# Performance work log

Measured on AMD Instinct MI355X. Metric: run time of the kernel, lower is better.

Reference implementation:

```python
import jax, jax.numpy as jnp
import numpy as np

D_MODEL = 2048
N_HEADS = 16
HEAD_DIM = D_MODEL // N_HEADS
ROPE_BASE = 10000.0


def rope_cos_sin(seq_len, head_dim, dtype=jnp.float32):
    inv_freq = 1.0 / (ROPE_BASE ** (jnp.arange(0, head_dim, 2, dtype=jnp.float32) / head_dim))
    pos = jnp.arange(seq_len, dtype=jnp.float32)
    freqs = pos[:, None] * inv_freq[None, :]          # [S, head_dim/2]
    emb = jnp.concatenate([freqs, freqs], axis=-1)    # [S, head_dim]
    return jnp.cos(emb).astype(dtype), jnp.sin(emb).astype(dtype)


def rotate_half(x):
    x1, x2 = jnp.split(x, 2, axis=-1)
    return jnp.concatenate([-x2, x1], axis=-1)


def apply_rope(x, cos, sin):
    # x: [B, S, H, hd]; cos/sin: [S, hd] broadcast over batch and heads
    c = cos[None, :, None, :]
    s = sin[None, :, None, :]
    return x * c + rotate_half(x) * s


def setup_inputs() -> dict:
    key = jax.random.key(0)
    kx, kq, kk, kv, ko = jax.random.split(key, 5)
    B, S = 4, 2048
    scale = 1.0 / np.sqrt(D_MODEL)
    x = jax.random.normal(kx, (B, S, D_MODEL), dtype=jnp.float32)
    Wq = jax.random.normal(kq, (D_MODEL, D_MODEL), dtype=jnp.float32) * scale
    Wk = jax.random.normal(kk, (D_MODEL, D_MODEL), dtype=jnp.float32) * scale
    Wv = jax.random.normal(kv, (D_MODEL, D_MODEL), dtype=jnp.float32) * scale
    Wo = jax.random.normal(ko, (D_MODEL, D_MODEL), dtype=jnp.float32) * scale
    return {"x": x, "Wq": Wq, "Wk": Wk, "Wv": Wv, "Wo": Wo}


def reference(x, Wq, Wk, Wv, Wo):
    B, S, D = x.shape
    H, hd = N_HEADS, HEAD_DIM
    # QKV projections (torch Linear: y = x @ W.T)
    q = jnp.einsum('bsd,ed->bse', x, Wq).reshape(B, S, H, hd)
    k = jnp.einsum('bsd,ed->bse', x, Wk).reshape(B, S, H, hd)
    v = jnp.einsum('bsd,ed->bse', x, Wv).reshape(B, S, H, hd)
    # RoPE (no past cache -> positions 0..S-1 for both Q and K)
    cos, sin = rope_cos_sin(S, hd, x.dtype)
    q = apply_rope(q, cos, sin)
    k = apply_rope(k, cos, sin)
    # Scaled dot-product attention, causal (training path with mask=None)
    scores = jnp.einsum('bqhd,bkhd->bhqk', q, k) / jnp.sqrt(jnp.asarray(hd, x.dtype))
    causal = jnp.tril(jnp.ones((S, S), dtype=bool))
    scores = jnp.where(causal[None, None], scores, jnp.asarray(-jnp.inf, scores.dtype))
    attn = jax.nn.softmax(scores, axis=-1)
    out = jnp.einsum('bhqk,bkhd->bqhd', attn, v).reshape(B, S, D)
    return jnp.einsum('bsd,ed->bse', out, Wo)
```

## Files before the change

kernel.cpp:

```cpp
#include <hip/hip_runtime.h>
#include <stdint.h>

#define DMODEL 2048
#define NHEADS 16
#define HD     128
#define BATCH  4
#define SEQ    2048
#define MROWS  (BATCH*SEQ)

typedef __attribute__((ext_vector_type(8))) short short8;
typedef __attribute__((ext_vector_type(4))) float f32x4;

__device__ __forceinline__ unsigned short f2bf(float f) {
  uint32_t u = __float_as_uint(f);
  u += 0x7FFFu + ((u >> 16) & 1u);
  return (unsigned short)(u >> 16);
}
__device__ __forceinline__ float bf2f(unsigned short s) {
  return __uint_as_float(((uint32_t)s) << 16);
}

__global__ __launch_bounds__(256) void cvt_f32_bf16(
    const float* __restrict__ src, unsigned short* __restrict__ dst, int n4) {
  int i = blockIdx.x * 256 + threadIdx.x;
  if (i >= n4) return;
  float4 f = ((const float4*)src)[i];
  ushort4 o;
  o.x = f2bf(f.x); o.y = f2bf(f.y); o.z = f2bf(f.z); o.w = f2bf(f.w);
  ((ushort4*)dst)[i] = o;
}

__global__ __launch_bounds__(256) void rope_table(
    float* __restrict__ ct, float* __restrict__ st) {
  int idx = blockIdx.x * 256 + threadIdx.x;
  int s = idx >> 6, i = idx & 63;
  float invf = exp2f(-(float)i * (13.287712379549449f / 64.0f));
  float a = (float)s * invf;
  ct[idx] = cosf(a);
  st[idx] = sinf(a);
}

__global__ __launch_bounds__(256) void rope_apply(
    unsigned short* __restrict__ X, const float* __restrict__ ct,
    const float* __restrict__ st) {
  int idx = blockIdx.x * 256 + threadIdx.x;
  int i0  = (idx & 15) * 4;
  int h   = (idx >> 4) & 15;
  int row = idx >> 8;
  int s   = row & (SEQ - 1);
  size_t base = (size_t)row * DMODEL + h * HD + i0;
  ushort4 lo = *(const ushort4*)&X[base];
  ushort4 hi = *(const ushort4*)&X[base + 64];
  float4 c  = *(const float4*)&ct[s * 64 + i0];
  float4 sn = *(const float4*)&st[s * 64 + i0];
  ushort4 olo, ohi;
  olo.x = f2bf(bf2f(lo.x) * c.x - bf2f(hi.x) * sn.x);
  olo.y = f2bf(bf2f(lo.y) * c.y - bf2f(hi.y) * sn.y);
  olo.z = f2bf(bf2f(lo.z) * c.z - bf2f(hi.z) * sn.z);
  olo.w = f2bf(bf2f(lo.w) * c.w - bf2f(hi.w) * sn.w);
  ohi.x = f2bf(bf2f(hi.x) * c.x + bf2f(lo.x) * sn.x);
  ohi.y = f2bf(bf2f(hi.y) * c.y + bf2f(lo.y) * sn.y);
  ohi.z = f2bf(bf2f(hi.z) * c.z + bf2f(lo.z) * sn.z);
  ohi.w = f2bf(bf2f(hi.w) * c.w + bf2f(lo.w) * sn.w);
  *(ushort4*)&X[base]      = olo;
  *(ushort4*)&X[base + 64] = ohi;
}

template<bool OUT_BF16>
__global__ __launch_bounds__(256) void gemm_nt(
    const unsigned short* __restrict__ A,
    const unsigned short* __restrict__ B0, const unsigned short* __restrict__ B1,
    const unsigned short* __restrict__ B2,
    void* __restrict__ C0, void* __restrict__ C1, void* __restrict__ C2,
    int K, int N) {
  const unsigned short* Bm = (blockIdx.z == 0) ? B0 : (blockIdx.z == 1) ? B1 : B2;
  void* Cm = (blockIdx.z == 0) ? C0 : (blockIdx.z == 1) ? C1 : C2;
  const int m0 = blockIdx.x * 128, n0 = blockIdx.y * 128;
  __shared__ unsigned short As[128 * 64];
  __shared__ unsigned short Bs[128 * 64];
  const int t = threadIdx.x, w = t >> 6, lane = t & 63;
  const int wr = w >> 1, wc = w & 1, g = lane >> 4, cl = lane & 15;

  f32x4 acc[4][4];
  const f32x4 zero = {0.f, 0.f, 0.f, 0.f};
#pragma unroll
  for (int mi = 0; mi < 4; ++mi)
#pragma unroll
    for (int ni = 0; ni < 4; ++ni) acc[mi][ni] = zero;

  for (int k0 = 0; k0 < K; k0 += 64) {
    __syncthreads();
#pragma unroll
    for (int i = 0; i < 4; ++i) {
      int f16 = (w * 4 + i) * 64 + lane;
      int row = f16 >> 3, col = (f16 & 7) * 8;
      __builtin_amdgcn_global_load_lds(
          (const __attribute__((address_space(1))) void*)(A + (size_t)(m0 + row) * K + k0 + col),
          (__attribute__((address_space(3))) void*)(&As[(size_t)f16 * 8]), 16, 0, 0);
      __builtin_amdgcn_global_load_lds(
          (const __attribute__((address_space(1))) void*)(Bm + (size_t)(n0 + row) * K + k0 + col),
          (__attribute__((address_space(3))) void*)(&Bs[(size_t)f16 * 8]), 16, 0, 0);
    }
    __syncthreads();
#pragma unroll
    for (int kk = 0; kk < 2; ++kk) {
      short8 a[4], b[4];
#pragma unroll
      for (int mi = 0; mi < 4; ++mi)
        a[mi] = *(const short8*)&As[(wr * 64 + mi * 16 + cl) * 64 + kk * 32 + g * 8];
#pragma unroll
      for (int ni = 0; ni < 4; ++ni)
        b[ni] = *(const short8*)&Bs[(wc * 64 + ni * 16 + cl) * 64 + kk * 32 + g * 8];
#pragma unroll
      for (int mi = 0; mi < 4; ++mi)
#pragma unroll
        for (int ni = 0; ni < 4; ++ni)
          acc[mi][ni] = __builtin_amdgcn_mfma_f32_16x16x32_bf16(a[mi], b[ni], acc[mi][ni], 0, 0, 0);
    }
  }
#pragma unroll
  for (int mi = 0; mi < 4; ++mi)
#pragma unroll
    for (int ni = 0; ni < 4; ++ni) {
      int row = m0 + wr * 64 + mi * 16 + g * 4;
      int col = n0 + wc * 64 + ni * 16 + cl;
#pragma unroll
      for (int r = 0; r < 4; ++r) {
        float v = acc[mi][ni][r];
        if (OUT_BF16)
          ((unsigned short*)Cm)[(size_t)(row + r) * N + col] = f2bf(v);
        else
          ((float*)Cm)[(size_t)(row + r) * N + col] = v;
      }
    }
}

__global__ __launch_bounds__(256) void attn_kernel(
    const unsigned short* __restrict__ Q, const unsigned short* __restrict__ Kk,
    const unsigned short* __restrict__ V, unsigned short* __restrict__ O) {
  const int qt = (int)gridDim.x - 1 - (int)blockIdx.x;
  const int q0 = qt * 64;
  const int bh = blockIdx.y, b = bh >> 4, h = bh & 15;
  const size_t base = (size_t)b * SEQ * DMODEL + (size_t)h * HD;

  __shared__ unsigned short Ks[64 * 136];
  __shared__ unsigned short Vt[128 * 72];
  __shared__ unsigned short Pl[4][16 * 72];

  const int t = threadIdx.x, w = t >> 6, lane = t & 63;
  const int g = lane >> 4, cl = lane & 15;

  short8 qf[4];
  {
    const unsigned short* qrow = Q + base + (size_t)(q0 + w * 16 + cl) * DMODEL;
#pragma unroll
    for (int kk = 0; kk < 4; ++kk) qf[kk] = *(const short8*)(qrow + kk * 32 + g * 8);
  }

  f32x4 o_acc[8];
  const f32x4 zero = {0.f, 0.f, 0.f, 0.f};
#pragma unroll
  for (int n = 0; n < 8; ++n) o_acc[n] = zero;
  float m_run[4], l_run[4];
#pragma unroll
  for (int r = 0; r < 4; ++r) { m_run[r] = -INFINITY; l_run[r] = 0.f; }

  const int my_qmax = q0 + w * 16 + 15;
  const int ntiles = qt + 1;
  constexpr float SC = 0.08838834764831845f * 1.4426950408889634f;

  for (int tkv = 0; tkv < ntiles; ++tkv) {
    const int kv0 = tkv * 64;
    __syncthreads();
#pragma unroll
    for (int p = 0; p < 4; ++p) {
      int row = p * 16 + (t >> 4), c8 = t & 15;
      const unsigned short* src = Kk + base + (size_t)(kv0 + row) * DMODEL + c8 * 8;
      *(short8*)&Ks[row * 136 + c8 * 8] = *(const short8*)src;
    }
#pragma unroll
    for (int p = 0; p < 4; ++p) {
      int kv = t & 63, h0 = ((t >> 6) + p * 4) * 8;
      const unsigned short* src = V + base + (size_t)(kv0 + kv) * DMODEL + h0;
      short8 vv = *(const short8*)src;
#pragma unroll
      for (int e = 0; e < 8; ++e) Vt[(h0 + e) * 72 + kv] = (unsigned short)vv[e];
    }
    __syncthreads();

    if (kv0 <= my_qmax) {
      float sm[4][4];
#pragma unroll
      for (int c = 0; c < 4; ++c) {
        f32x4 sa = zero;
#pragma unroll
        for (int kk = 0; kk < 4; ++kk) {
          short8 kf = *(const short8*)&Ks[(c * 16 + cl) * 136 + kk * 32 + g * 8];
          sa = __builtin_amdgcn_mfma_f32_16x16x32_bf16(qf[kk], kf, sa, 0, 0, 0);
        }
#pragma unroll
        for (int r = 0; r < 4; ++r) {
          float sv = sa[r] * SC;
          int kvg = kv0 + c * 16 + cl;
          int qg  = q0 + w * 16 + g * 4 + r;
          sm[c][r] = (kvg > qg) ? -INFINITY : sv;
        }
      }
      float alpha[4];
#pragma unroll
      for (int r = 0; r < 4; ++r) {
        float mx = fmaxf(fmaxf(sm[0][r], sm[1][r]), fmaxf(sm[2][r], sm[3][r]));
#pragma unroll
        for (int msk = 8; msk >= 1; msk >>= 1) mx = fmaxf(mx, __shfl_xor(mx, msk, 16));
        float mnew = fmaxf(m_run[r], mx);
        alpha[r] = exp2f(m_run[r] - mnew);
        m_run[r] = mnew;
        float s0 = 0.f;
#pragma unroll
        for (int c = 0; c < 4; ++c) {
          float p = exp2f(sm[c][r] - mnew);
          sm[c][r] = p;
          s0 += p;
        }
#pragma unroll
        for (int msk = 8; msk >= 1; msk >>= 1) s0 += __shfl_xor(s0, msk, 16);
        l_run[r] = l_run[r] * alpha[r] + s0;
      }
#pragma unroll
      for (int n = 0; n < 8; ++n)
#pragma unroll
        for (int r = 0; r < 4; ++r) o_acc[n][r] *= alpha[r];
#pragma unroll
      for (int c = 0; c < 4; ++c)
#pragma unroll
        for (int r = 0; r < 4; ++r)
          Pl[w][(g * 4 + r) * 72 + c * 16 + cl] = f2bf(sm[c][r]);
#pragma unroll
      for (int kk = 0; kk < 2; ++kk) {
        short8 pa = *(const short8*)&Pl[w][cl * 72 + kk * 32 + g * 8];
#pragma unroll
        for (int n = 0; n < 8; ++n) {
          short8 vf = *(const short8*)&Vt[(n * 16 + cl) * 72 + kk * 32 + g * 8];
          o_acc[n] = __builtin_amdgcn_mfma_f32_16x16x32_bf16(pa, vf, o_acc[n], 0, 0, 0);
        }
      }
    }
  }
  {
    const size_t obase = base + (size_t)(q0 + w * 16) * DMODEL;
#pragma unroll
    for (int r = 0; r < 4; ++r) {
      float inv = 1.0f / l_run[r];
      int qrow = g * 4 + r;
#pragma unroll
      for (int n = 0; n < 8; ++n)
        O[obase + (size_t)qrow * DMODEL + n * 16 + cl] = f2bf(o_acc[n][r] * inv);
    }
  }
}

extern "C" void kernel_launch(void* const* d_in, const int* in_sizes, int n_in,
                              void* d_out, int out_size, void* d_ws, size_t ws_size,
                              hipStream_t stream) {
  const float* x  = (const float*)d_in[0];
  const float* Wq = (const float*)d_in[1];
  const float* Wk = (const float*)d_in[2];
  const float* Wv = (const float*)d_in[3];
  const float* Wo = (const float*)d_in[4];
  float* out = (float*)d_out;

  unsigned short* wsb = (unsigned short*)d_ws;
  const size_t XN = (size_t)MROWS * DMODEL;
  const size_t WN = (size_t)DMODEL * DMODEL;
  unsigned short* xb  = wsb;
  unsigned short* wqb = xb  + XN;
  unsigned short* wkb = wqb + WN;
  unsigned short* wvb = wkb + WN;
  unsigned short* wob = wvb + WN;
  unsigned short* qb  = wob + WN;
  unsigned short* kb  = qb  + XN;
  unsigned short* vb  = kb  + XN;
  unsigned short* aob = vb  + XN;
  float* cost = (float*)(aob + XN);
  float* sint = cost + (size_t)SEQ * 64;

  cvt_f32_bf16<<<(int)(XN / 4 / 256), 256, 0, stream>>>(x,  xb,  (int)(XN / 4));
  cvt_f32_bf16<<<(int)(WN / 4 / 256), 256, 0, stream>>>(Wq, wqb, (int)(WN / 4));
  cvt_f32_bf16<<<(int)(WN / 4 / 256), 256, 0, stream>>>(Wk, wkb, (int)(WN / 4));
  cvt_f32_bf16<<<(int)(WN / 4 / 256), 256, 0, stream>>>(Wv, wvb, (int)(WN / 4));
  cvt_f32_bf16<<<(int)(WN / 4 / 256), 256, 0, stream>>>(Wo, wob, (int)(WN / 4));

  rope_table<<<(SEQ * 64) / 256, 256, 0, stream>>>(cost, sint);

  gemm_nt<true><<<dim3(MROWS / 128, DMODEL / 128, 3), 256, 0, stream>>>(
      xb, wqb, wkb, wvb, (void*)qb, (void*)kb, (void*)vb, DMODEL, DMODEL);

  rope_apply<<<(MROWS * NHEADS * 16) / 256, 256, 0, stream>>>(qb, cost, sint);
  rope_apply<<<(MROWS * NHEADS * 16) / 256, 256, 0, stream>>>(kb, cost, sint);

  attn_kernel<<<dim3(SEQ / 64, BATCH * NHEADS), 256, 0, stream>>>(qb, kb, vb, aob);

  gemm_nt<false><<<dim3(MROWS / 128, DMODEL / 128, 1), 256, 0, stream>>>(
      aob, wob, wob, wob, (void*)out, (void*)out, (void*)out, DMODEL, DMODEL);
}
```

Measured before the change: 996.8 us.

## Pre-transpose V, use direct global-to-LDS loads with swizzle, double Q tile

Adds a separate kernel that transposes V into a per-head [hd, S] layout, stored in the reused x buffer. The attention kernel then loads K and V^T tiles with global_load_lds directly into XOR-swizzled LDS instead of scattering per element. It also moves to 512 threads and 128-row Q tiles, so each K/V tile load is shared by twice as many waves. The aim is to cut LDS bank conflicts, the per-element V transpose, and redundant global K/V traffic, at the cost of one extra kernel pass over V and possibly lower occupancy.

```diff
diff --git a/kernel.cpp b/kernel.cpp
--- a/kernel.cpp
+++ b/kernel.cpp
@@ -135,17 +135,48 @@
     }
 }
 
-__global__ __launch_bounds__(256) void attn_kernel(
+__global__ __launch_bounds__(256) void transpose_v(
+    const unsigned short* __restrict__ Vin, unsigned short* __restrict__ Vt) {
+  const int s0 = blockIdx.x * 128;
+  const int bh = blockIdx.y, b = bh >> 4, h = bh & 15;
+  __shared__ unsigned short Ts[128 * 136];
+  const int t = threadIdx.x;
+  const unsigned short* src = Vin + ((size_t)b * SEQ + s0) * DMODEL + h * HD;
+#pragma unroll
+  for (int p = 0; p < 8; ++p) {
+    int task = t + p * 256;
+    int r = task >> 4, ch = task & 15;
+    *(short8*)&Ts[r * 136 + ch * 8] = *(const short8*)(src + (size_t)r * DMODEL + ch * 8);
+  }
+  __syncthreads();
+  unsigned short* dst = Vt + ((size_t)bh << 18) + s0;
+#pragma unroll
+  for (int p = 0; p < 2; ++p) {
+    int task = t + p * 256;
+    int d = task & 127, csq = task >> 7;
+#pragma unroll
+    for (int j = 0; j < 4; ++j) {
+      short8 v;
+#pragma unroll
+      for (int e = 0; e < 8; ++e)
+        v[e] = (short)Ts[(csq * 32 + j * 8 + e) * 136 + d];
+      *(short8*)(dst + (size_t)d * SEQ + csq * 32 + j * 8) = v;
+    }
+  }
+}
+
+__global__ __launch_bounds__(512) void attn_kernel(
     const unsigned short* __restrict__ Q, const unsigned short* __restrict__ Kk,
-    const unsigned short* __restrict__ V, unsigned short* __restrict__ O) {
+    const unsigned short* __restrict__ Vt, unsigned short* __restrict__ O) {
   const int qt = (int)gridDim.x - 1 - (int)blockIdx.x;
-  const int q0 = qt * 64;
+  const int q0 = qt * 128;
   const int bh = blockIdx.y, b = bh >> 4, h = bh & 15;
   const size_t base = (size_t)b * SEQ * DMODEL + (size_t)h * HD;
-
-  __shared__ unsigned short Ks[64 * 136];
-  __shared__ unsigned short Vt[128 * 72];
-  __shared__ unsigned short Pl[4][16 * 72];
+  const unsigned short* vbase = Vt + ((size_t)bh << 18);
+
+  __shared__ unsigned short Ks[64 * 128];
+  __shared__ unsigned short Vs[128 * 64];
+  __shared__ unsigned short Pl[8 * 16 * 64];
 
   const int t = threadIdx.x, w = t >> 6, lane = t & 63;
   const int g = lane >> 4, cl = lane & 15;
@@ -166,25 +197,25 @@
   for (int r = 0; r < 4; ++r) { m_run[r] = -INFINITY; l_run[r] = 0.f; }
 
   const int my_qmax = q0 + w * 16 + 15;
-  const int ntiles = qt + 1;
+  const int ntiles = 2 * qt + 2;
   constexpr float SC = 0.08838834764831845f * 1.4426950408889634f;
 
   for (int tkv = 0; tkv < ntiles; ++tkv) {
     const int kv0 = tkv * 64;
     __syncthreads();
 #pragma unroll
-    for (int p = 0; p < 4; ++p) {
-      int row = p * 16 + (t >> 4), c8 = t & 15;
-      const unsigned short* src = Kk + base + (size_t)(kv0 + row) * DMODEL + c8 * 8;
-      *(short8*)&Ks[row * 136 + c8 * 8] = *(const short8*)src;
-    }
-#pragma unroll
-    for (int p = 0; p < 4; ++p) {
-      int kv = t & 63, h0 = ((t >> 6) + p * 4) * 8;
-      const unsigned short* src = V + base + (size_t)(kv0 + kv) * DMODEL + h0;
-      short8 vv = *(const short8*)src;
-#pragma unroll
-      for (int e = 0; e < 8; ++e) Vt[(h0 + e) * 72 + kv] = (unsigned short)vv[e];
+    for (int p = 0; p < 2; ++p) {
+      int ck = p * 512 + t;
+      int kr = ck >> 4, kc = ck & 15;
+      int kcg = kc ^ (kr & 7);
+      __builtin_amdgcn_global_load_lds(
+          (const __attribute__((address_space(1))) void*)(Kk + base + (size_t)(kv0 + kr) * DMODEL + kcg * 8),
+          (__attribute__((address_space(3))) void*)(&Ks[ck * 8]), 16, 0, 0);
+      int vd = ck >> 3, vc = ck & 7;
+      int vcg = vc ^ (vd & 7);
+      __builtin_amdgcn_global_load_lds(
+          (const __attribute__((address_space(1))) void*)(vbase + (size_t)vd * SEQ + kv0 + vcg * 8),
+          (__attribute__((address_space(3))) void*)(&Vs[ck * 8]), 16, 0, 0);
     }
     __syncthreads();
 
@@ -195,7 +226,7 @@
         f32x4 sa = zero;
 #pragma unroll
         for (int kk = 0; kk < 4; ++kk) {
-          short8 kf = *(const short8*)&Ks[(c * 16 + cl) * 136 + kk * 32 + g * 8];
+          short8 kf = *(const short8*)&Ks[(c * 16 + cl) * 128 + (((kk * 4 + g) ^ (cl & 7)) << 3)];
           sa = __builtin_amdgcn_mfma_f32_16x16x32_bf16(qf[kk], kf, sa, 0, 0, 0);
         }
 #pragma unroll
@@ -233,14 +264,17 @@
 #pragma unroll
       for (int c = 0; c < 4; ++c)
 #pragma unroll
-        for (int r = 0; r < 4; ++r)
-          Pl[w][(g * 4 + r) * 72 + c * 16 + cl] = f2bf(sm[c][r]);
+        for (int r = 0; r < 4; ++r) {
+          int q = g * 4 + r;
+          int chs = ((c * 2 + (cl >> 3)) ^ (q & 7)) << 3;
+          Pl[w * 1024 + q * 64 + chs + (cl & 7)] = f2bf(sm[c][r]);
+        }
 #pragma unroll
       for (int kk = 0; kk < 2; ++kk) {
-        short8 pa = *(const short8*)&Pl[w][cl * 72 + kk * 32 + g * 8];
+        short8 pa = *(const short8*)&Pl[w * 1024 + cl * 64 + (((kk * 4 + g) ^ (cl & 7)) << 3)];
 #pragma unroll
         for (int n = 0; n < 8; ++n) {
-          short8 vf = *(const short8*)&Vt[(n * 16 + cl) * 72 + kk * 32 + g * 8];
+          short8 vf = *(const short8*)&Vs[(n * 16 + cl) * 64 + (((kk * 4 + g) ^ (cl & 7)) << 3)];
           o_acc[n] = __builtin_amdgcn_mfma_f32_16x16x32_bf16(pa, vf, o_acc[n], 0, 0, 0);
         }
       }
@@ -283,6 +317,7 @@
   unsigned short* aob = vb  + XN;
   float* cost = (float*)(aob + XN);
   float* sint = cost + (size_t)SEQ * 64;
+  unsigned short* vtg = xb;
 
   cvt_f32_bf16<<<(int)(XN / 4 / 256), 256, 0, stream>>>(x,  xb,  (int)(XN / 4));
   cvt_f32_bf16<<<(int)(WN / 4 / 256), 256, 0, stream>>>(Wq, wqb, (int)(WN / 4));
@@ -295,10 +330,12 @@
   gemm_nt<true><<<dim3(MROWS / 128, DMODEL / 128, 3), 256, 0, stream>>>(
       xb, wqb, wkb, wvb, (void*)qb, (void*)kb, (void*)vb, DMODEL, DMODEL);
 
+  transpose_v<<<dim3(SEQ / 128, BATCH * NHEADS), 256, 0, stream>>>(vb, vtg);
+
   rope_apply<<<(MROWS * NHEADS * 16) / 256, 256, 0, stream>>>(qb, cost, sint);
   rope_apply<<<(MROWS * NHEADS * 16) / 256, 256, 0, stream>>>(kb, cost, sint);
 
-  attn_kernel<<<dim3(SEQ / 64, BATCH * NHEADS), 256, 0, stream>>>(qb, kb, vb, aob);
+  attn_kernel<<<dim3(SEQ / 128, BATCH * NHEADS), 512, 0, stream>>>(qb, kb, vtg, aob);
 
   gemm_nt<false><<<dim3(MROWS / 128, DMODEL / 128, 1), 256, 0, stream>>>(
       aob, wob, wob, wob, (void*)out, (void*)out, (void*)out, DMODEL, DMODEL);
```

After: 957.3 us. 4.0% less time.
